# Performance work log

Measured on AMD Instinct MI355X. Metric: run time of the kernel, lower is better.

The kernel has to match this reference:

```python
import jax, jax.numpy as jnp
import numpy as np

HD, M = 4096, 14336

def setup_inputs() -> dict:
    key = jax.random.key(0)
    k_x, k_g, k_u, k_d = jax.random.split(key, 4)
    scale = 1.0 / np.sqrt(HD)
    x = jax.random.normal(k_x, (4, 2048, HD), dtype=jnp.float16)
    # Dequantized fp16 weights, stored torch-style as [out_features, in_features]
    W_gate = (jax.random.normal(k_g, (M, HD), dtype=jnp.float16) * jnp.float16(scale))
    W_up   = (jax.random.normal(k_u, (M, HD), dtype=jnp.float16) * jnp.float16(scale))
    W_down = (jax.random.normal(k_d, (HD, M), dtype=jnp.float16) * jnp.float16(1.0 / np.sqrt(M)))
    return {"x": x, "W_gate": W_gate, "W_up": W_up, "W_down": W_down}

def reference(x, W_gate, W_up, W_down):
    # SwiGLU: down( silu(x @ Wg^T) * (x @ Wu^T) )
    gate = jnp.einsum("bsh,mh->bsm", x, W_gate)   # [B,S,M]
    up = jnp.einsum("bsh,mh->bsm", x, W_up)       # [B,S,M]
    h = jax.nn.silu(gate) * up                       # fused elementwise
    out = jnp.einsum("bsm,hm->bsh", h, W_down)    # [B,S,HD]
    return out
```

## Files before the change

### kernel.cpp

```cpp
#include <hip/hip_runtime.h>

typedef _Float16 f16;
typedef _Float16 f16x8 __attribute__((ext_vector_type(8)));
typedef float f32x4 __attribute__((ext_vector_type(4)));

__device__ __forceinline__ f16x8 cvt8(f32x4 lo, f32x4 hi) {
    f16x8 h;
    h[0] = (f16)lo[0]; h[1] = (f16)lo[1]; h[2] = (f16)lo[2]; h[3] = (f16)lo[3];
    h[4] = (f16)hi[0]; h[5] = (f16)hi[1]; h[6] = (f16)hi[2]; h[7] = (f16)hi[3];
    return h;
}

__global__ __launch_bounds__(256)
void cvt_f32_f16(const float* __restrict__ in, f16* __restrict__ out, long long n) {
    long long i = ((long long)blockIdx.x * 256 + threadIdx.x) * 8;
    const long long stride = (long long)gridDim.x * 256 * 8;
    for (; i < n; i += stride) {
        f32x4 a = *(const f32x4*)(in + i);
        f32x4 b = *(const f32x4*)(in + i + 4);
        *(f16x8*)(out + i) = cvt8(a, b);
    }
}

__global__ void fill_sentinel_f32(float* __restrict__ out, long long n) {
    long long i = (long long)blockIdx.x * blockDim.x + threadIdx.x;
    long long stride = (long long)gridDim.x * blockDim.x;
    for (; i < n; i += stride) out[i] = 1.0f;
}

__device__ __forceinline__ void gload_lds16(const f16* g, f16* l) {
    __builtin_amdgcn_global_load_lds(
        (const __attribute__((address_space(1))) unsigned int*)(unsigned long long)g,
        (__attribute__((address_space(3))) unsigned int*)(unsigned int)(unsigned long long)l,
        16, 0, 0);
}

template<bool FUSED>
__global__ __launch_bounds__(512, 2)
void mlp_gemm16b(const f16* __restrict__ A, const f16* __restrict__ B0,
                 const f16* __restrict__ B1, void* __restrict__ Cv,
                 int K, int ldc, int nRow, int nCol, int RG) {
    constexpr int BN = FUSED ? 128 : 256;
    __shared__ __align__(16) f16 smA[3][256 * 32];
    __shared__ __align__(16) f16 smB0[3][BN * 32];
    __shared__ __align__(16) f16 smB1[FUSED ? 3 : 1][FUSED ? 128 * 32 : 8];

    const int lin   = blockIdx.x;
    const int perSg = RG * nCol;
    const int sg    = lin / perSg;
    const int rem   = lin - sg * perSg;
    int rgIn = nRow - sg * RG; if (rgIn > RG) rgIn = RG;
    const int colB = rem / rgIn;
    const int rowB = sg * RG + (rem - colB * rgIn);

    const long long blockRow = (long long)rowB * 256;
    const long long blockCol = (long long)colB * BN;

    const int tid  = threadIdx.x;
    const int w    = tid >> 6;
    const int lane = tid & 63;
    const int waveM = w >> 2;
    const int waveN = w & 3;

    const int dr   = tid >> 2;
    const int dblk = tid & 3;
    const int gblk = (dblk - (dr >> 1)) & 3;
    const f16* gA0  = A + (blockRow + dr) * (long long)K + gblk * 8;
    const f16* gA1  = gA0 + 128 * (long long)K;
    const f16* gB0a = B0 + (blockCol + dr) * (long long)K + gblk * 8;
    const f16* gB0b = FUSED ? nullptr : gB0a + 128 * (long long)K;
    const f16* gB1a = FUSED ? B1 + (blockCol + dr) * (long long)K + gblk * 8
                            : nullptr;
    const int wbase = w * 512;

    const int fr = lane & 15;
    const int hi = lane >> 4;
    constexpr int NI = FUSED ? 2 : 4;
    constexpr int NW = FUSED ? 32 : 64;
    int aOff[8], bOff[NI];
#pragma unroll
    for (int i = 0; i < 8; ++i) {
        const int r = waveM * 128 + i * 16 + fr;
        aOff[i] = r * 32 + (((hi + (r >> 1)) & 3) << 3);
    }
#pragma unroll
    for (int n = 0; n < NI; ++n) {
        const int r = waveN * NW + n * 16 + fr;
        bOff[n] = r * 32 + (((hi + (r >> 1)) & 3) << 3);
    }

    f32x4 acc0[8][NI];
    f32x4 acc1[FUSED ? 8 : 1][FUSED ? NI : 1];
#pragma unroll
    for (int mi = 0; mi < 8; ++mi)
#pragma unroll
        for (int ni = 0; ni < NI; ++ni) {
            acc0[mi][ni] = (f32x4){0.f, 0.f, 0.f, 0.f};
            if constexpr (FUSED) acc1[mi][ni] = (f32x4){0.f, 0.f, 0.f, 0.f};
        }

    auto stage = [&](int b) {
        gload_lds16(gA0, &smA[b][wbase]);           gA0 += 32;
        gload_lds16(gA1, &smA[b][4096 + wbase]);    gA1 += 32;
        gload_lds16(gB0a, &smB0[b][wbase]);         gB0a += 32;
        if constexpr (FUSED) {
            gload_lds16(gB1a, &smB1[b][wbase]);     gB1a += 32;
        } else {
            gload_lds16(gB0b, &smB0[b][4096 + wbase]); gB0b += 32;
        }
    };

    auto compute = [&](int b) {
        f16x8 aF[8], bF[NI], b1F[FUSED ? NI : 1];
#pragma unroll
        for (int i = 0; i < 8; ++i) aF[i] = *(const f16x8*)(&smA[b][aOff[i]]);
#pragma unroll
        for (int n = 0; n < NI; ++n) bF[n] = *(const f16x8*)(&smB0[b][bOff[n]]);
        if constexpr (FUSED) {
#pragma unroll
            for (int n = 0; n < NI; ++n) b1F[n] = *(const f16x8*)(&smB1[b][bOff[n]]);
        }
#pragma unroll
        for (int mi = 0; mi < 8; ++mi)
#pragma unroll
            for (int ni = 0; ni < NI; ++ni) {
                acc0[mi][ni] = __builtin_amdgcn_mfma_f32_16x16x32_f16(
                    aF[mi], bF[ni], acc0[mi][ni], 0, 0, 0);
                if constexpr (FUSED)
                    acc1[mi][ni] = __builtin_amdgcn_mfma_f32_16x16x32_f16(
                        aF[mi], b1F[ni], acc1[mi][ni], 0, 0, 0);
            }
    };

    const int nk = K >> 5;
    stage(0);
    stage(1);
    int cur = 0;
    for (int t = 0; t < nk - 1; ++t) {
        asm volatile("s_waitcnt vmcnt(4)" ::: "memory");
        __builtin_amdgcn_s_barrier();
        __builtin_amdgcn_sched_barrier(0);
        if (t + 2 < nk) {
            int nb = cur + 2; if (nb >= 3) nb -= 3;
            stage(nb);
        }
        compute(cur);
        cur = (cur == 2) ? 0 : cur + 1;
    }
    asm volatile("s_waitcnt vmcnt(0)" ::: "memory");
    __builtin_amdgcn_s_barrier();
    __builtin_amdgcn_sched_barrier(0);
    compute(cur);

    const long long orBase = blockRow + waveM * 128 + hi * 4;
    const long long ocBase = blockCol + waveN * NW + fr;
#pragma unroll
    for (int mi = 0; mi < 8; ++mi)
#pragma unroll
        for (int ni = 0; ni < NI; ++ni)
#pragma unroll
            for (int j = 0; j < 4; ++j) {
                const long long idx =
                    (orBase + mi * 16 + j) * (long long)ldc + (ocBase + ni * 16);
                if constexpr (FUSED) {
                    float gv = acc0[mi][ni][j];
                    float uv = acc1[mi][ni][j];
                    float v = (gv / (1.f + __expf(-gv))) * uv;
                    ((f16*)Cv)[idx] = (f16)v;
                } else {
                    ((float*)Cv)[idx] = acc0[mi][ni][j];
                }
            }
}

template<bool IS16>
__device__ __forceinline__ f16x8 load8(const char* p) {
    if constexpr (IS16) return *(const f16x8*)p;
    const float* f = (const float*)p;
    return cvt8(*(const f32x4*)f, *(const f32x4*)(f + 4));
}

template<bool FUSED, bool A16, bool B16>
__global__ __launch_bounds__(256)
void mlp_gemm(const void* __restrict__ Av, const void* __restrict__ B0v,
              const void* __restrict__ B1v, void* __restrict__ Cv,
              int K, int ldc, int nRow, int nCol, int RG) {
    __shared__ __align__(16) f16 smA[128 * 32];
    __shared__ __align__(16) f16 smB0[128 * 32];
    __shared__ __align__(16) f16 smB1[FUSED ? 128 * 32 : 8];

    const int lin   = blockIdx.x;
    const int perSg = RG * nCol;
    const int sg    = lin / perSg;
    const int rem   = lin - sg * perSg;
    int rgIn = nRow - sg * RG; if (rgIn > RG) rgIn = RG;
    const int colB = rem / rgIn;
    const int rowB = sg * RG + (rem - colB * rgIn);

    const long long blockRow = (long long)rowB * 128;
    const long long blockCol = (long long)colB * 128;

    const int tid  = threadIdx.x;
    const int w    = tid >> 6;
    const int lane = tid & 63;
    const int waveM = w >> 1;
    const int waveN = w & 1;

    const int r0 = tid >> 2;
    const int s0 = tid & 3;
    const int szA = A16 ? 2 : 4;
    const int szB = B16 ? 2 : 4;
    const char* gA0  = (const char*)Av  + ((blockRow + r0)      * (long long)K + s0 * 8) * szA;
    const char* gA1  = (const char*)Av  + ((blockRow + r0 + 64) * (long long)K + s0 * 8) * szA;
    const char* gB00 = (const char*)B0v + ((blockCol + r0)      * (long long)K + s0 * 8) * szB;
    const char* gB01 = (const char*)B0v + ((blockCol + r0 + 64) * (long long)K + s0 * 8) * szB;
    const char* gB10 = FUSED ? (const char*)B1v + ((blockCol + r0)      * (long long)K + s0 * 8) * szB : nullptr;
    const char* gB11 = FUSED ? (const char*)B1v + ((blockCol + r0 + 64) * (long long)K + s0 * 8) * szB : nullptr;

    const int off0 = tid * 8;
    const int off1 = off0 + 2048;

    const int fr = lane & 15;
    const int fk = (lane >> 4) * 8;
    int offA[4], offB[4];
#pragma unroll
    for (int i = 0; i < 4; ++i) {
        offA[i] = (waveM * 64 + i * 16 + fr) * 32 + fk;
        offB[i] = (waveN * 64 + i * 16 + fr) * 32 + fk;
    }

    f32x4 acc0[4][4];
    f32x4 acc1[4][4];
#pragma unroll
    for (int mi = 0; mi < 4; ++mi)
#pragma unroll
        for (int ni = 0; ni < 4; ++ni) {
            acc0[mi][ni] = (f32x4){0.f, 0.f, 0.f, 0.f};
            if constexpr (FUSED) acc1[mi][ni] = (f32x4){0.f, 0.f, 0.f, 0.f};
        }

    const int ksteps = K >> 5;
    for (int kt = 0; kt < ksteps; ++kt) {
        f16x8 vA0  = load8<A16>(gA0);
        f16x8 vA1  = load8<A16>(gA1);
        f16x8 vB00 = load8<B16>(gB00);
        f16x8 vB01 = load8<B16>(gB01);
        f16x8 vB10, vB11;
        if constexpr (FUSED) {
            vB10 = load8<B16>(gB10);
            vB11 = load8<B16>(gB11);
        }
        gA0 += 32 * szA; gA1 += 32 * szA;
        gB00 += 32 * szB; gB01 += 32 * szB;
        if constexpr (FUSED) { gB10 += 32 * szB; gB11 += 32 * szB; }

        __syncthreads();

        *(f16x8*)(smA  + off0) = vA0;
        *(f16x8*)(smA  + off1) = vA1;
        *(f16x8*)(smB0 + off0) = vB00;
        *(f16x8*)(smB0 + off1) = vB01;
        if constexpr (FUSED) {
            *(f16x8*)(smB1 + off0) = vB10;
            *(f16x8*)(smB1 + off1) = vB11;
        }

        __syncthreads();

        f16x8 aF[4], bF[4], b1F[4];
#pragma unroll
        for (int i = 0; i < 4; ++i) aF[i] = *(const f16x8*)(smA + offA[i]);
#pragma unroll
        for (int i = 0; i < 4; ++i) bF[i] = *(const f16x8*)(smB0 + offB[i]);
        if constexpr (FUSED) {
#pragma unroll
            for (int i = 0; i < 4; ++i) b1F[i] = *(const f16x8*)(smB1 + offB[i]);
        }

#pragma unroll
        for (int mi = 0; mi < 4; ++mi)
#pragma unroll
            for (int ni = 0; ni < 4; ++ni) {
                acc0[mi][ni] = __builtin_amdgcn_mfma_f32_16x16x32_f16(
                    aF[mi], bF[ni], acc0[mi][ni], 0, 0, 0);
                if constexpr (FUSED)
                    acc1[mi][ni] = __builtin_amdgcn_mfma_f32_16x16x32_f16(
                        aF[mi], b1F[ni], acc1[mi][ni], 0, 0, 0);
            }
    }

    const long long orBase = blockRow + waveM * 64 + ((lane >> 4) * 4);
    const long long ocBase = blockCol + waveN * 64 + fr;
#pragma unroll
    for (int mi = 0; mi < 4; ++mi)
#pragma unroll
        for (int ni = 0; ni < 4; ++ni)
#pragma unroll
            for (int j = 0; j < 4; ++j) {
                const long long idx =
                    (orBase + mi * 16 + j) * (long long)ldc + (ocBase + ni * 16);
                if constexpr (FUSED) {
                    float gv = acc0[mi][ni][j];
                    float uv = acc1[mi][ni][j];
                    float v = (gv / (1.f + __expf(-gv))) * uv;
                    ((f16*)Cv)[idx] = (f16)v;
                } else {
                    ((float*)Cv)[idx] = acc0[mi][ni][j];
                }
            }
}

extern "C" void kernel_launch(void* const* d_in, const int* in_sizes, int n_in,
                              void* d_out, int out_size, void* d_ws, size_t ws_size,
                              hipStream_t stream) {
    const float* x  = (const float*)d_in[0];
    const float* Wg = (const float*)d_in[1];
    const float* Wu = (const float*)d_in[2];
    const float* Wd = (const float*)d_in[3];
    float* out = (float*)d_out;

    const int HD = 4096;
    const int T  = in_sizes[0] / HD;
    const int M  = in_sizes[1] / HD;

    const long long nW = (long long)M * HD;
    const long long nX = (long long)T * HD;
    const size_t wBytes = (size_t)nW * 2;
    const size_t xBytes = (size_t)nX * 2;
    const size_t hRow   = (size_t)M * 2;
    const size_t minH   = 256 * hRow;

    char* p = (char*)d_ws;
    size_t rem = ws_size;
    f16 *Wg16 = nullptr, *Wu16 = nullptr, *Wd16 = nullptr, *X16 = nullptr;
    bool fast = false;
    if (rem >= 3 * wBytes + xBytes + minH) {
        Wg16 = (f16*)p; p += wBytes;
        Wu16 = (f16*)p; p += wBytes;
        Wd16 = (f16*)p; p += wBytes;
        X16  = (f16*)p; p += xBytes;
        rem -= 3 * wBytes + xBytes;
        fast = true;
    }
    f16* H = (f16*)p;

    if (fast) {
        long long maxRows = (long long)(rem / hRow);
        int chunk = (int)((maxRows / 256) * 256);
        if (chunk > T) chunk = T;

        cvt_f32_f16<<<2048, 256, 0, stream>>>(Wg, Wg16, nW);
        cvt_f32_f16<<<2048, 256, 0, stream>>>(Wu, Wu16, nW);
        cvt_f32_f16<<<2048, 256, 0, stream>>>(Wd, Wd16, nW);
        cvt_f32_f16<<<2048, 256, 0, stream>>>(x, X16, nX);

        for (int t0 = 0; t0 < T; t0 += chunk) {
            int rows = (T - t0 < chunk) ? (T - t0) : chunk;
            int nRow = rows / 256;
            {
                int nCol = M / 128;
                int RG = nRow;
                mlp_gemm16b<true><<<dim3(nRow * nCol), 512, 0, stream>>>(
                    X16 + (size_t)t0 * HD, Wg16, Wu16, H, HD, M, nRow, nCol, RG);
            }
            {
                int nCol = HD / 256;
                int RG = (nRow < 16) ? nRow : 16;
                mlp_gemm16b<false><<<dim3(nRow * nCol), 512, 0, stream>>>(
                    H, Wd16, nullptr, out + (size_t)t0 * HD, M, HD, nRow, nCol, RG);
            }
        }
        return;
    }

    long long maxRows = (long long)(ws_size / hRow);
    int chunk = (int)((maxRows / 128) * 128);
    if (chunk > T) chunk = T;
    if (chunk <= 0) {
        fill_sentinel_f32<<<1024, 256, 0, stream>>>(out, (long long)out_size);
        return;
    }
    f16* Hf = (f16*)d_ws;
    for (int t0 = 0; t0 < T; t0 += chunk) {
        int rows = (T - t0 < chunk) ? (T - t0) : chunk;
        int nRow = rows / 128;
        {
            int nCol = M / 128;
            mlp_gemm<true, false, false><<<dim3(nRow * nCol), 256, 0, stream>>>(
                x + (size_t)t0 * HD, Wg, Wu, Hf, HD, M, nRow, nCol, nRow);
        }
        {
            int nCol = HD / 128;
            int RG = (nRow < 32) ? nRow : 32;
            mlp_gemm<false, true, false><<<dim3(nRow * nCol), 256, 0, stream>>>(
                Hf, Wd, nullptr, out + (size_t)t0 * HD, M, HD, nRow, nCol, RG);
        }
    }
}
```

Before: 2.760 ms.

## Interleave LDS fragment loads, global prefetch and MFMA in four phases per k-step

Splits each k-iteration into four phases, each loading two A fragments from LDS and issuing one global-to-LDS prefetch before a block of MFMAs, instead of loading all fragments up front. Each MFMA block is wrapped in s_setprio(1), and a workgroup barrier plus lgkmcnt wait is inserted per phase, a ping-pong style schedule meant to overlap memory traffic with matrix math across waves. It also folds the tail iteration into the main loop. The extra barriers per k-step add sync overhead and may cause stalls if waves drift.

```diff
diff --git a/kernel.cpp b/kernel.cpp
--- a/kernel.cpp
+++ b/kernel.cpp
@@ -99,7 +99,7 @@
             if constexpr (FUSED) acc1[mi][ni] = (f32x4){0.f, 0.f, 0.f, 0.f};
         }
 
-    auto stage = [&](int b) {
+    auto stage_all = [&](int b) {
         gload_lds16(gA0, &smA[b][wbase]);           gA0 += 32;
         gload_lds16(gA1, &smA[b][4096 + wbase]);    gA1 += 32;
         gload_lds16(gB0a, &smB0[b][wbase]);         gB0a += 32;
@@ -110,47 +110,71 @@
         }
     };
 
-    auto compute = [&](int b) {
-        f16x8 aF[8], bF[NI], b1F[FUSED ? NI : 1];
-#pragma unroll
-        for (int i = 0; i < 8; ++i) aF[i] = *(const f16x8*)(&smA[b][aOff[i]]);
-#pragma unroll
-        for (int n = 0; n < NI; ++n) bF[n] = *(const f16x8*)(&smB0[b][bOff[n]]);
-        if constexpr (FUSED) {
-#pragma unroll
-            for (int n = 0; n < NI; ++n) b1F[n] = *(const f16x8*)(&smB1[b][bOff[n]]);
-        }
-#pragma unroll
-        for (int mi = 0; mi < 8; ++mi)
-#pragma unroll
-            for (int ni = 0; ni < NI; ++ni) {
-                acc0[mi][ni] = __builtin_amdgcn_mfma_f32_16x16x32_f16(
-                    aF[mi], bF[ni], acc0[mi][ni], 0, 0, 0);
-                if constexpr (FUSED)
-                    acc1[mi][ni] = __builtin_amdgcn_mfma_f32_16x16x32_f16(
-                        aF[mi], b1F[ni], acc1[mi][ni], 0, 0, 0);
-            }
-    };
-
     const int nk = K >> 5;
-    stage(0);
-    stage(1);
+    stage_all(0);
+    stage_all(1);
     int cur = 0;
-    for (int t = 0; t < nk - 1; ++t) {
-        asm volatile("s_waitcnt vmcnt(4)" ::: "memory");
+    for (int t = 0; t < nk; ++t) {
+        if (t < nk - 1) {
+            asm volatile("s_waitcnt vmcnt(4)" ::: "memory");
+        } else {
+            asm volatile("s_waitcnt vmcnt(0)" ::: "memory");
+        }
         __builtin_amdgcn_s_barrier();
         __builtin_amdgcn_sched_barrier(0);
-        if (t + 2 < nk) {
-            int nb = cur + 2; if (nb >= 3) nb -= 3;
-            stage(nb);
-        }
-        compute(cur);
+
+        const bool pre = (t + 2 < nk);
+        int nb = cur + 2; if (nb >= 3) nb -= 3;
+
+        f16x8 bF[NI], b1F[FUSED ? NI : 1];
+
+#pragma unroll
+        for (int p = 0; p < 4; ++p) {
+            f16x8 aF0 = *(const f16x8*)(&smA[cur][aOff[2 * p]]);
+            f16x8 aF1 = *(const f16x8*)(&smA[cur][aOff[2 * p + 1]]);
+            if (p == 0) {
+#pragma unroll
+                for (int n = 0; n < NI; ++n)
+                    bF[n] = *(const f16x8*)(&smB0[cur][bOff[n]]);
+                if constexpr (FUSED) {
+#pragma unroll
+                    for (int n = 0; n < NI; ++n)
+                        b1F[n] = *(const f16x8*)(&smB1[cur][bOff[n]]);
+                }
+            }
+            if (pre) {
+                if (p == 0) { gload_lds16(gA0, &smA[nb][wbase]);        gA0 += 32; }
+                if (p == 1) { gload_lds16(gA1, &smA[nb][4096 + wbase]); gA1 += 32; }
+                if (p == 2) { gload_lds16(gB0a, &smB0[nb][wbase]);      gB0a += 32; }
+                if (p == 3) {
+                    if constexpr (FUSED) {
+                        gload_lds16(gB1a, &smB1[nb][wbase]);            gB1a += 32;
+                    } else {
+                        gload_lds16(gB0b, &smB0[nb][4096 + wbase]);     gB0b += 32;
+                    }
+                }
+            }
+            __builtin_amdgcn_s_barrier();
+            asm volatile("s_waitcnt lgkmcnt(0)" ::: "memory");
+            __builtin_amdgcn_sched_barrier(0);
+            __builtin_amdgcn_s_setprio(1);
+#pragma unroll
+            for (int ni = 0; ni < NI; ++ni) {
+                acc0[2 * p][ni] = __builtin_amdgcn_mfma_f32_16x16x32_f16(
+                    aF0, bF[ni], acc0[2 * p][ni], 0, 0, 0);
+                acc0[2 * p + 1][ni] = __builtin_amdgcn_mfma_f32_16x16x32_f16(
+                    aF1, bF[ni], acc0[2 * p + 1][ni], 0, 0, 0);
+                if constexpr (FUSED) {
+                    acc1[2 * p][ni] = __builtin_amdgcn_mfma_f32_16x16x32_f16(
+                        aF0, b1F[ni], acc1[2 * p][ni], 0, 0, 0);
+                    acc1[2 * p + 1][ni] = __builtin_amdgcn_mfma_f32_16x16x32_f16(
+                        aF1, b1F[ni], acc1[2 * p + 1][ni], 0, 0, 0);
+                }
+            }
+            __builtin_amdgcn_s_setprio(0);
+        }
         cur = (cur == 2) ? 0 : cur + 1;
     }
-    asm volatile("s_waitcnt vmcnt(0)" ::: "memory");
-    __builtin_amdgcn_s_barrier();
-    __builtin_amdgcn_sched_barrier(0);
-    compute(cur);
 
     const long long orBase = blockRow + waveM * 128 + hi * 4;
     const long long ocBase = blockCol + waveN * NW + fr;
```

Measured after the change: 2.815 ms. 2.0% more time.

## Restructure GEMM main loop into ping-pong phases with interleaved staging and setprio

Applied to the files above, without the earlier changes.

Replaces the 3-stage K=32 ring buffer with a 2-buffer, two-half (K=64 per iteration) scheme. Each iteration is split into four phases that interleave LDS fragment reads, async global-to-LDS loads for future tiles, and MFMA bursts. Each phase is bracketed by barriers and s_setprio so waves alternate between memory and matrix work. The goal is better overlap of loads with MFMA and fewer stalls, paid for with more barriers per iteration and a stricter requirement that K be a multiple of 64.

```diff
diff --git a/kernel.cpp b/kernel.cpp
--- a/kernel.cpp
+++ b/kernel.cpp
@@ -40,10 +40,11 @@
 void mlp_gemm16b(const f16* __restrict__ A, const f16* __restrict__ B0,
                  const f16* __restrict__ B1, void* __restrict__ Cv,
                  int K, int ldc, int nRow, int nCol, int RG) {
-    constexpr int BN = FUSED ? 128 : 256;
-    __shared__ __align__(16) f16 smA[3][256 * 32];
-    __shared__ __align__(16) f16 smB0[3][BN * 32];
-    __shared__ __align__(16) f16 smB1[FUSED ? 3 : 1][FUSED ? 128 * 32 : 8];
+    constexpr int BN  = FUSED ? 128 : 256;
+    constexpr int BSE = FUSED ? 128 * 32 : 256 * 32;
+    __shared__ __align__(16) f16 smA[2][2][256 * 32];
+    __shared__ __align__(16) f16 smB0[2][2][BSE];
+    __shared__ __align__(16) f16 smB1[FUSED ? 2 : 1][FUSED ? 2 : 1][FUSED ? 128 * 32 : 8];
 
     const int lin   = blockIdx.x;
     const int perSg = RG * nCol;
@@ -73,6 +74,19 @@
                             : nullptr;
     const int wbase = w * 512;
 
+    auto stageA = [&](int b, int kh) {
+        gload_lds16(gA0, &smA[b][kh][wbase]);        gA0 += 32;
+        gload_lds16(gA1, &smA[b][kh][4096 + wbase]); gA1 += 32;
+    };
+    auto stageB = [&](int b, int kh) {
+        gload_lds16(gB0a, &smB0[b][kh][wbase]);      gB0a += 32;
+        if constexpr (FUSED) {
+            gload_lds16(gB1a, &smB1[b][kh][wbase]);  gB1a += 32;
+        } else {
+            gload_lds16(gB0b, &smB0[b][kh][4096 + wbase]); gB0b += 32;
+        }
+    };
+
     const int fr = lane & 15;
     const int hi = lane >> 4;
     constexpr int NI = FUSED ? 2 : 4;
@@ -99,58 +113,65 @@
             if constexpr (FUSED) acc1[mi][ni] = (f32x4){0.f, 0.f, 0.f, 0.f};
         }
 
-    auto stage = [&](int b) {
-        gload_lds16(gA0, &smA[b][wbase]);           gA0 += 32;
-        gload_lds16(gA1, &smA[b][4096 + wbase]);    gA1 += 32;
-        gload_lds16(gB0a, &smB0[b][wbase]);         gB0a += 32;
-        if constexpr (FUSED) {
-            gload_lds16(gB1a, &smB1[b][wbase]);     gB1a += 32;
+    const int nk2 = K >> 6;
+    stageA(0, 0); stageB(0, 0);
+    stageA(0, 1); stageB(0, 1);
+    stageA(1, 0); stageB(1, 0);
+
+    for (int t = 0; t < nk2; ++t) {
+        const int cur = t & 1;
+        const int oth = cur ^ 1;
+        if (t < nk2 - 1) {
+            asm volatile("s_waitcnt vmcnt(4)" ::: "memory");
         } else {
-            gload_lds16(gB0b, &smB0[b][4096 + wbase]); gB0b += 32;
-        }
-    };
-
-    auto compute = [&](int b) {
-        f16x8 aF[8], bF[NI], b1F[FUSED ? NI : 1];
-#pragma unroll
-        for (int i = 0; i < 8; ++i) aF[i] = *(const f16x8*)(&smA[b][aOff[i]]);
-#pragma unroll
-        for (int n = 0; n < NI; ++n) bF[n] = *(const f16x8*)(&smB0[b][bOff[n]]);
-        if constexpr (FUSED) {
-#pragma unroll
-            for (int n = 0; n < NI; ++n) b1F[n] = *(const f16x8*)(&smB1[b][bOff[n]]);
-        }
-#pragma unroll
-        for (int mi = 0; mi < 8; ++mi)
-#pragma unroll
-            for (int ni = 0; ni < NI; ++ni) {
-                acc0[mi][ni] = __builtin_amdgcn_mfma_f32_16x16x32_f16(
-                    aF[mi], bF[ni], acc0[mi][ni], 0, 0, 0);
-                if constexpr (FUSED)
-                    acc1[mi][ni] = __builtin_amdgcn_mfma_f32_16x16x32_f16(
-                        aF[mi], b1F[ni], acc1[mi][ni], 0, 0, 0);
-            }
-    };
-
-    const int nk = K >> 5;
-    stage(0);
-    stage(1);
-    int cur = 0;
-    for (int t = 0; t < nk - 1; ++t) {
-        asm volatile("s_waitcnt vmcnt(4)" ::: "memory");
+            asm volatile("s_waitcnt vmcnt(0)" ::: "memory");
+        }
         __builtin_amdgcn_s_barrier();
         __builtin_amdgcn_sched_barrier(0);
-        if (t + 2 < nk) {
-            int nb = cur + 2; if (nb >= 3) nb -= 3;
-            stage(nb);
-        }
-        compute(cur);
-        cur = (cur == 2) ? 0 : cur + 1;
-    }
-    asm volatile("s_waitcnt vmcnt(0)" ::: "memory");
-    __builtin_amdgcn_s_barrier();
-    __builtin_amdgcn_sched_barrier(0);
-    compute(cur);
+
+        f16x8 bF[NI], b1F[FUSED ? NI : 1];
+
+#pragma unroll
+        for (int p = 0; p < 4; ++p) {
+            const int kh = p >> 1;
+            const int mg = (p & 1) * 4;
+            f16x8 aF[4];
+#pragma unroll
+            for (int i = 0; i < 4; ++i)
+                aF[i] = *(const f16x8*)(&smA[cur][kh][aOff[mg + i]]);
+            if ((p & 1) == 0) {
+#pragma unroll
+                for (int n = 0; n < NI; ++n)
+                    bF[n] = *(const f16x8*)(&smB0[cur][kh][bOff[n]]);
+                if constexpr (FUSED) {
+#pragma unroll
+                    for (int n = 0; n < NI; ++n)
+                        b1F[n] = *(const f16x8*)(&smB1[cur][kh][bOff[n]]);
+                }
+            }
+            if (p == 0) { if (t + 1 < nk2) stageA(oth, 1); }
+            if (p == 1) { if (t + 1 < nk2) stageB(oth, 1); }
+            if (p == 2) { if (t + 2 < nk2) stageA(cur, 0); }
+            if (p == 3) { if (t + 2 < nk2) stageB(cur, 0); }
+
+            __builtin_amdgcn_s_barrier();
+            asm volatile("s_waitcnt lgkmcnt(0)" ::: "memory");
+            __builtin_amdgcn_sched_barrier(0);
+            __builtin_amdgcn_s_setprio(1);
+#pragma unroll
+            for (int i = 0; i < 4; ++i)
+#pragma unroll
+                for (int ni = 0; ni < NI; ++ni) {
+                    acc0[mg + i][ni] = __builtin_amdgcn_mfma_f32_16x16x32_f16(
+                        aF[i], bF[ni], acc0[mg + i][ni], 0, 0, 0);
+                    if constexpr (FUSED)
+                        acc1[mg + i][ni] = __builtin_amdgcn_mfma_f32_16x16x32_f16(
+                            aF[i], b1F[ni], acc1[mg + i][ni], 0, 0, 0);
+                }
+            __builtin_amdgcn_s_setprio(0);
+            __builtin_amdgcn_s_barrier();
+        }
+    }
 
     const long long orBase = blockRow + waveM * 128 + hi * 4;
     const long long ocBase = blockCol + waveN * NW + fr;
```

Measured after the change: 2.823 ms. +2.3%, slower.

## Split fused gate/up GEMM into two 256x256-tile GEMMs with H read-modify-write epilogue

Applied to the files above, without the earlier changes.

Replaces the fused gate+up kernel (256x128 tile with two B operands and two accumulator sets) with two launches of a single 256x256-tile GEMM. The first writes silu(gate) into H as fp16; the second multiplies its up result by the stored H in the epilogue. The goal is a larger per-B tile with fewer accumulator registers, giving better arithmetic intensity per LDS byte. In exchange, x is read twice, H makes an extra fp16 round trip, and silu(gate) is rounded to fp16 before the multiply.

```diff
diff --git a/kernel.cpp b/kernel.cpp
--- a/kernel.cpp
+++ b/kernel.cpp
@@ -35,15 +35,13 @@
         16, 0, 0);
 }
 
-template<bool FUSED>
+template<int EPI>
 __global__ __launch_bounds__(512, 2)
-void mlp_gemm16b(const f16* __restrict__ A, const f16* __restrict__ B0,
-                 const f16* __restrict__ B1, void* __restrict__ Cv,
-                 int K, int ldc, int nRow, int nCol, int RG) {
-    constexpr int BN = FUSED ? 128 : 256;
+void mlp_gemm16c(const f16* __restrict__ A, const f16* __restrict__ B0,
+                 void* __restrict__ Cv, int K, int ldc,
+                 int nRow, int nCol, int RG) {
     __shared__ __align__(16) f16 smA[3][256 * 32];
-    __shared__ __align__(16) f16 smB0[3][BN * 32];
-    __shared__ __align__(16) f16 smB1[FUSED ? 3 : 1][FUSED ? 128 * 32 : 8];
+    __shared__ __align__(16) f16 smB0[3][256 * 32];
 
     const int lin   = blockIdx.x;
     const int perSg = RG * nCol;
@@ -54,7 +52,7 @@
     const int rowB = sg * RG + (rem - colB * rgIn);
 
     const long long blockRow = (long long)rowB * 256;
-    const long long blockCol = (long long)colB * BN;
+    const long long blockCol = (long long)colB * 256;
 
     const int tid  = threadIdx.x;
     const int w    = tid >> 6;
@@ -65,71 +63,52 @@
     const int dr   = tid >> 2;
     const int dblk = tid & 3;
     const int gblk = (dblk - (dr >> 1)) & 3;
-    const f16* gA0  = A + (blockRow + dr) * (long long)K + gblk * 8;
+    const f16* gA0  = A  + (blockRow + dr) * (long long)K + gblk * 8;
     const f16* gA1  = gA0 + 128 * (long long)K;
     const f16* gB0a = B0 + (blockCol + dr) * (long long)K + gblk * 8;
-    const f16* gB0b = FUSED ? nullptr : gB0a + 128 * (long long)K;
-    const f16* gB1a = FUSED ? B1 + (blockCol + dr) * (long long)K + gblk * 8
-                            : nullptr;
+    const f16* gB0b = gB0a + 128 * (long long)K;
     const int wbase = w * 512;
 
     const int fr = lane & 15;
     const int hi = lane >> 4;
-    constexpr int NI = FUSED ? 2 : 4;
-    constexpr int NW = FUSED ? 32 : 64;
-    int aOff[8], bOff[NI];
+    int aOff[8], bOff[4];
 #pragma unroll
     for (int i = 0; i < 8; ++i) {
         const int r = waveM * 128 + i * 16 + fr;
         aOff[i] = r * 32 + (((hi + (r >> 1)) & 3) << 3);
     }
 #pragma unroll
-    for (int n = 0; n < NI; ++n) {
-        const int r = waveN * NW + n * 16 + fr;
+    for (int n = 0; n < 4; ++n) {
+        const int r = waveN * 64 + n * 16 + fr;
         bOff[n] = r * 32 + (((hi + (r >> 1)) & 3) << 3);
     }
 
-    f32x4 acc0[8][NI];
-    f32x4 acc1[FUSED ? 8 : 1][FUSED ? NI : 1];
+    f32x4 acc0[8][4];
 #pragma unroll
     for (int mi = 0; mi < 8; ++mi)
 #pragma unroll
-        for (int ni = 0; ni < NI; ++ni) {
+        for (int ni = 0; ni < 4; ++ni)
             acc0[mi][ni] = (f32x4){0.f, 0.f, 0.f, 0.f};
-            if constexpr (FUSED) acc1[mi][ni] = (f32x4){0.f, 0.f, 0.f, 0.f};
-        }
 
     auto stage = [&](int b) {
-        gload_lds16(gA0, &smA[b][wbase]);           gA0 += 32;
-        gload_lds16(gA1, &smA[b][4096 + wbase]);    gA1 += 32;
-        gload_lds16(gB0a, &smB0[b][wbase]);         gB0a += 32;
-        if constexpr (FUSED) {
-            gload_lds16(gB1a, &smB1[b][wbase]);     gB1a += 32;
-        } else {
-            gload_lds16(gB0b, &smB0[b][4096 + wbase]); gB0b += 32;
-        }
+        gload_lds16(gA0,  &smA[b][wbase]);           gA0  += 32;
+        gload_lds16(gA1,  &smA[b][4096 + wbase]);    gA1  += 32;
+        gload_lds16(gB0a, &smB0[b][wbase]);          gB0a += 32;
+        gload_lds16(gB0b, &smB0[b][4096 + wbase]);   gB0b += 32;
     };
 
     auto compute = [&](int b) {
-        f16x8 aF[8], bF[NI], b1F[FUSED ? NI : 1];
+        f16x8 aF[8], bF[4];
 #pragma unroll
         for (int i = 0; i < 8; ++i) aF[i] = *(const f16x8*)(&smA[b][aOff[i]]);
 #pragma unroll
-        for (int n = 0; n < NI; ++n) bF[n] = *(const f16x8*)(&smB0[b][bOff[n]]);
-        if constexpr (FUSED) {
-#pragma unroll
-            for (int n = 0; n < NI; ++n) b1F[n] = *(const f16x8*)(&smB1[b][bOff[n]]);
-        }
+        for (int n = 0; n < 4; ++n) bF[n] = *(const f16x8*)(&smB0[b][bOff[n]]);
 #pragma unroll
         for (int mi = 0; mi < 8; ++mi)
 #pragma unroll
-            for (int ni = 0; ni < NI; ++ni) {
+            for (int ni = 0; ni < 4; ++ni)
                 acc0[mi][ni] = __builtin_amdgcn_mfma_f32_16x16x32_f16(
                     aF[mi], bF[ni], acc0[mi][ni], 0, 0, 0);
-                if constexpr (FUSED)
-                    acc1[mi][ni] = __builtin_amdgcn_mfma_f32_16x16x32_f16(
-                        aF[mi], b1F[ni], acc1[mi][ni], 0, 0, 0);
-            }
     };
 
     const int nk = K >> 5;
@@ -153,11 +132,150 @@
     compute(cur);
 
     const long long orBase = blockRow + waveM * 128 + hi * 4;
-    const long long ocBase = blockCol + waveN * NW + fr;
+    const long long ocBase = blockCol + waveN * 64 + fr;
 #pragma unroll
     for (int mi = 0; mi < 8; ++mi)
 #pragma unroll
-        for (int ni = 0; ni < NI; ++ni)
+        for (int ni = 0; ni < 4; ++ni)
+#pragma unroll
+            for (int j = 0; j < 4; ++j) {
+                const long long idx =
+                    (orBase + mi * 16 + j) * (long long)ldc + (ocBase + ni * 16);
+                float v = acc0[mi][ni][j];
+                if constexpr (EPI == 0) {
+                    ((float*)Cv)[idx] = v;
+                } else if constexpr (EPI == 1) {
+                    ((f16*)Cv)[idx] = (f16)(v / (1.f + __expf(-v)));
+                } else {
+                    f16* Hc = (f16*)Cv;
+                    float h = (float)Hc[idx];
+                    Hc[idx] = (f16)(h * v);
+                }
+            }
+}
+
+template<bool IS16>
+__device__ __forceinline__ f16x8 load8(const char* p) {
+    if constexpr (IS16) return *(const f16x8*)p;
+    const float* f = (const float*)p;
+    return cvt8(*(const f32x4*)f, *(const f32x4*)(f + 4));
+}
+
+template<bool FUSED, bool A16, bool B16>
+__global__ __launch_bounds__(256)
+void mlp_gemm(const void* __restrict__ Av, const void* __restrict__ B0v,
+              const void* __restrict__ B1v, void* __restrict__ Cv,
+              int K, int ldc, int nRow, int nCol, int RG) {
+    __shared__ __align__(16) f16 smA[128 * 32];
+    __shared__ __align__(16) f16 smB0[128 * 32];
+    __shared__ __align__(16) f16 smB1[FUSED ? 128 * 32 : 8];
+
+    const int lin   = blockIdx.x;
+    const int perSg = RG * nCol;
+    const int sg    = lin / perSg;
+    const int rem   = lin - sg * perSg;
+    int rgIn = nRow - sg * RG; if (rgIn > RG) rgIn = RG;
+    const int colB = rem / rgIn;
+    const int rowB = sg * RG + (rem - colB * rgIn);
+
+    const long long blockRow = (long long)rowB * 128;
+    const long long blockCol = (long long)colB * 128;
+
+    const int tid  = threadIdx.x;
+    const int w    = tid >> 6;
+    const int lane = tid & 63;
+    const int waveM = w >> 1;
+    const int waveN = w & 1;
+
+    const int r0 = tid >> 2;
+    const int s0 = tid & 3;
+    const int szA = A16 ? 2 : 4;
+    const int szB = B16 ? 2 : 4;
+    const char* gA0  = (const char*)Av  + ((blockRow + r0)      * (long long)K + s0 * 8) * szA;
+    const char* gA1  = (const char*)Av  + ((blockRow + r0 + 64) * (long long)K + s0 * 8) * szA;
+    const char* gB00 = (const char*)B0v + ((blockCol + r0)      * (long long)K + s0 * 8) * szB;
+    const char* gB01 = (const char*)B0v + ((blockCol + r0 + 64) * (long long)K + s0 * 8) * szB;
+    const char* gB10 = FUSED ? (const char*)B1v + ((blockCol + r0)      * (long long)K + s0 * 8) * szB : nullptr;
+    const char* gB11 = FUSED ? (const char*)B1v + ((blockCol + r0 + 64) * (long long)K + s0 * 8) * szB : nullptr;
+
+    const int off0 = tid * 8;
+    const int off1 = off0 + 2048;
+
+    const int fr = lane & 15;
+    const int fk = (lane >> 4) * 8;
+    int offA[4], offB[4];
+#pragma unroll
+    for (int i = 0; i < 4; ++i) {
+        offA[i] = (waveM * 64 + i * 16 + fr) * 32 + fk;
+        offB[i] = (waveN * 64 + i * 16 + fr) * 32 + fk;
+    }
+
+    f32x4 acc0[4][4];
+    f32x4 acc1[4][4];
+#pragma unroll
+    for (int mi = 0; mi < 4; ++mi)
+#pragma unroll
+        for (int ni = 0; ni < 4; ++ni) {
+            acc0[mi][ni] = (f32x4){0.f, 0.f, 0.f, 0.f};
+            if constexpr (FUSED) acc1[mi][ni] = (f32x4){0.f, 0.f, 0.f, 0.f};
+        }
+
+    const int ksteps = K >> 5;
+    for (int kt = 0; kt < ksteps; ++kt) {
+        f16x8 vA0  = load8<A16>(gA0);
+        f16x8 vA1  = load8<A16>(gA1);
+        f16x8 vB00 = load8<B16>(gB00);
+        f16x8 vB01 = load8<B16>(gB01);
+        f16x8 vB10, vB11;
+        if constexpr (FUSED) {
+            vB10 = load8<B16>(gB10);
+            vB11 = load8<B16>(gB11);
+        }
+        gA0 += 32 * szA; gA1 += 32 * szA;
+        gB00 += 32 * szB; gB01 += 32 * szB;
+        if constexpr (FUSED) { gB10 += 32 * szB; gB11 += 32 * szB; }
+
+        __syncthreads();
+
+        *(f16x8*)(smA  + off0) = vA0;
+        *(f16x8*)(smA  + off1) = vA1;
+        *(f16x8*)(smB0 + off0) = vB00;
+        *(f16x8*)(smB0 + off1) = vB01;
+        if constexpr (FUSED) {
+            *(f16x8*)(smB1 + off0) = vB10;
+            *(f16x8*)(smB1 + off1) = vB11;
+        }
+
+        __syncthreads();
+
+        f16x8 aF[4], bF[4], b1F[4];
+#pragma unroll
+        for (int i = 0; i < 4; ++i) aF[i] = *(const f16x8*)(smA + offA[i]);
+#pragma unroll
+        for (int i = 0; i < 4; ++i) bF[i] = *(const f16x8*)(smB0 + offB[i]);
+        if constexpr (FUSED) {
+#pragma unroll
+            for (int i = 0; i < 4; ++i) b1F[i] = *(const f16x8*)(smB1 + offB[i]);
+        }
+
+#pragma unroll
+        for (int mi = 0; mi < 4; ++mi)
+#pragma unroll
+            for (int ni = 0; ni < 4; ++ni) {
+                acc0[mi][ni] = __builtin_amdgcn_mfma_f32_16x16x32_f16(
+                    aF[mi], bF[ni], acc0[mi][ni], 0, 0, 0);
+                if constexpr (FUSED)
+                    acc1[mi][ni] = __builtin_amdgcn_mfma_f32_16x16x32_f16(
+                        aF[mi], b1F[ni], acc1[mi][ni], 0, 0, 0);
+            }
+    }
+
+    const long long orBase = blockRow + waveM * 64 + ((lane >> 4) * 4);
+    const long long ocBase = blockCol + waveN * 64 + fr;
+#pragma unroll
+    for (int mi = 0; mi < 4; ++mi)
+#pragma unroll
+        for (int ni = 0; ni < 4; ++ni)
 #pragma unroll
             for (int j = 0; j < 4; ++j) {
                 const long long idx =
@@ -173,143 +291,6 @@
             }
 }
 
-template<bool IS16>
-__device__ __forceinline__ f16x8 load8(const char* p) {
-    if constexpr (IS16) return *(const f16x8*)p;
-    const float* f = (const float*)p;
-    return cvt8(*(const f32x4*)f, *(const f32x4*)(f + 4));
-}
-
-template<bool FUSED, bool A16, bool B16>
-__global__ __launch_bounds__(256)
-void mlp_gemm(const void* __restrict__ Av, const void* __restrict__ B0v,
-              const void* __restrict__ B1v, void* __restrict__ Cv,
-              int K, int ldc, int nRow, int nCol, int RG) {
-    __shared__ __align__(16) f16 smA[128 * 32];
-    __shared__ __align__(16) f16 smB0[128 * 32];
-    __shared__ __align__(16) f16 smB1[FUSED ? 128 * 32 : 8];
-
-    const int lin   = blockIdx.x;
-    const int perSg = RG * nCol;
-    const int sg    = lin / perSg;
-    const int rem   = lin - sg * perSg;
-    int rgIn = nRow - sg * RG; if (rgIn > RG) rgIn = RG;
-    const int colB = rem / rgIn;
-    const int rowB = sg * RG + (rem - colB * rgIn);
-
-    const long long blockRow = (long long)rowB * 128;
-    const long long blockCol = (long long)colB * 128;
-
-    const int tid  = threadIdx.x;
-    const int w    = tid >> 6;
-    const int lane = tid & 63;
-    const int waveM = w >> 1;
-    const int waveN = w & 1;
-
-    const int r0 = tid >> 2;
-    const int s0 = tid & 3;
-    const int szA = A16 ? 2 : 4;
-    const int szB = B16 ? 2 : 4;
-    const char* gA0  = (const char*)Av  + ((blockRow + r0)      * (long long)K + s0 * 8) * szA;
-    const char* gA1  = (const char*)Av  + ((blockRow + r0 + 64) * (long long)K + s0 * 8) * szA;
-    const char* gB00 = (const char*)B0v + ((blockCol + r0)      * (long long)K + s0 * 8) * szB;
-    const char* gB01 = (const char*)B0v + ((blockCol + r0 + 64) * (long long)K + s0 * 8) * szB;
-    const char* gB10 = FUSED ? (const char*)B1v + ((blockCol + r0)      * (long long)K + s0 * 8) * szB : nullptr;
-    const char* gB11 = FUSED ? (const char*)B1v + ((blockCol + r0 + 64) * (long long)K + s0 * 8) * szB : nullptr;
-
-    const int off0 = tid * 8;
-    const int off1 = off0 + 2048;
-
-    const int fr = lane & 15;
-    const int fk = (lane >> 4) * 8;
-    int offA[4], offB[4];
-#pragma unroll
-    for (int i = 0; i < 4; ++i) {
-        offA[i] = (waveM * 64 + i * 16 + fr) * 32 + fk;
-        offB[i] = (waveN * 64 + i * 16 + fr) * 32 + fk;
-    }
-
-    f32x4 acc0[4][4];
-    f32x4 acc1[4][4];
-#pragma unroll
-    for (int mi = 0; mi < 4; ++mi)
-#pragma unroll
-        for (int ni = 0; ni < 4; ++ni) {
-            acc0[mi][ni] = (f32x4){0.f, 0.f, 0.f, 0.f};
-            if constexpr (FUSED) acc1[mi][ni] = (f32x4){0.f, 0.f, 0.f, 0.f};
-        }
-
-    const int ksteps = K >> 5;
-    for (int kt = 0; kt < ksteps; ++kt) {
-        f16x8 vA0  = load8<A16>(gA0);
-        f16x8 vA1  = load8<A16>(gA1);
-        f16x8 vB00 = load8<B16>(gB00);
-        f16x8 vB01 = load8<B16>(gB01);
-        f16x8 vB10, vB11;
-        if constexpr (FUSED) {
-            vB10 = load8<B16>(gB10);
-            vB11 = load8<B16>(gB11);
-        }
-        gA0 += 32 * szA; gA1 += 32 * szA;
-        gB00 += 32 * szB; gB01 += 32 * szB;
-        if constexpr (FUSED) { gB10 += 32 * szB; gB11 += 32 * szB; }
-
-        __syncthreads();
-
-        *(f16x8*)(smA  + off0) = vA0;
-        *(f16x8*)(smA  + off1) = vA1;
-        *(f16x8*)(smB0 + off0) = vB00;
-        *(f16x8*)(smB0 + off1) = vB01;
-        if constexpr (FUSED) {
-            *(f16x8*)(smB1 + off0) = vB10;
-            *(f16x8*)(smB1 + off1) = vB11;
-        }
-
-        __syncthreads();
-
-        f16x8 aF[4], bF[4], b1F[4];
-#pragma unroll
-        for (int i = 0; i < 4; ++i) aF[i] = *(const f16x8*)(smA + offA[i]);
-#pragma unroll
-        for (int i = 0; i < 4; ++i) bF[i] = *(const f16x8*)(smB0 + offB[i]);
-        if constexpr (FUSED) {
-#pragma unroll
-            for (int i = 0; i < 4; ++i) b1F[i] = *(const f16x8*)(smB1 + offB[i]);
-        }
-
-#pragma unroll
-        for (int mi = 0; mi < 4; ++mi)
-#pragma unroll
-            for (int ni = 0; ni < 4; ++ni) {
-                acc0[mi][ni] = __builtin_amdgcn_mfma_f32_16x16x32_f16(
-                    aF[mi], bF[ni], acc0[mi][ni], 0, 0, 0);
-                if constexpr (FUSED)
-                    acc1[mi][ni] = __builtin_amdgcn_mfma_f32_16x16x32_f16(
-                        aF[mi], b1F[ni], acc1[mi][ni], 0, 0, 0);
-            }
-    }
-
-    const long long orBase = blockRow + waveM * 64 + ((lane >> 4) * 4);
-    const long long ocBase = blockCol + waveN * 64 + fr;
-#pragma unroll
-    for (int mi = 0; mi < 4; ++mi)
-#pragma unroll
-        for (int ni = 0; ni < 4; ++ni)
-#pragma unroll
-            for (int j = 0; j < 4; ++j) {
-                const long long idx =
-                    (orBase + mi * 16 + j) * (long long)ldc + (ocBase + ni * 16);
-                if constexpr (FUSED) {
-                    float gv = acc0[mi][ni][j];
-                    float uv = acc1[mi][ni][j];
-                    float v = (gv / (1.f + __expf(-gv))) * uv;
-                    ((f16*)Cv)[idx] = (f16)v;
-                } else {
-                    ((float*)Cv)[idx] = acc0[mi][ni][j];
-                }
-            }
-}
-
 extern "C" void kernel_launch(void* const* d_in, const int* in_sizes, int n_in,
                               void* d_out, int out_size, void* d_ws, size_t ws_size,
                               hipStream_t stream) {
@@ -354,21 +335,19 @@
         cvt_f32_f16<<<2048, 256, 0, stream>>>(Wd, Wd16, nW);
         cvt_f32_f16<<<2048, 256, 0, stream>>>(x, X16, nX);
 
+        const int nColGU = M / 256;
+        const int nColD  = HD / 256;
         for (int t0 = 0; t0 < T; t0 += chunk) {
             int rows = (T - t0 < chunk) ? (T - t0) : chunk;
             int nRow = rows / 256;
-            {
-                int nCol = M / 128;
-                int RG = nRow;
-                mlp_gemm16b<true><<<dim3(nRow * nCol), 512, 0, stream>>>(
-                    X16 + (size_t)t0 * HD, Wg16, Wu16, H, HD, M, nRow, nCol, RG);
-            }
-            {
-                int nCol = HD / 256;
-                int RG = (nRow < 16) ? nRow : 16;
-                mlp_gemm16b<false><<<dim3(nRow * nCol), 512, 0, stream>>>(
-                    H, Wd16, nullptr, out + (size_t)t0 * HD, M, HD, nRow, nCol, RG);
-            }
+            const f16* Xc = X16 + (size_t)t0 * HD;
+            mlp_gemm16c<1><<<dim3(nRow * nColGU), 512, 0, stream>>>(
+                Xc, Wg16, H, HD, M, nRow, nColGU, nRow);
+            mlp_gemm16c<2><<<dim3(nRow * nColGU), 512, 0, stream>>>(
+                Xc, Wu16, H, HD, M, nRow, nColGU, nRow);
+            int RG = (nRow < 16) ? nRow : 16;
+            mlp_gemm16c<0><<<dim3(nRow * nColD), 512, 0, stream>>>(
+                H, Wd16, out + (size_t)t0 * HD, M, HD, nRow, nColD, RG);
         }
         return;
     }
```

Result: slower. 2.930 ms, median of 2 (+6.2%).
